# Kernel optimization log

Measured on AMD Instinct MI355X. Metric: run time of the kernel, lower is better.

Reference implementation:

```python
import jax, jax.numpy as jnp
import numpy as np


def _lambertw_real(z: float) -> float:
    # real branch W0 for z > e, Newton iteration (static, numpy)
    w = np.log(z) - np.log(np.log(z))
    for _ in range(30):
        ew = np.exp(w)
        w = w - (w * ew - z) / (ew * (w + 1.0))
    return float(w)


def setup_inputs() -> dict:
    key = jax.random.key(0)
    ks = jax.random.split(key, 8)
    B, D, Wd, Hd, heads = 4, 64, 48, 48, 4
    dh = D // heads
    return {
        "x": jax.random.normal(ks[0], (B, D, Wd, Hd), jnp.float32),
        "Wq": jax.random.normal(ks[1], (heads, dh, D), jnp.float32) * 0.05,
        "bq": jax.random.normal(ks[2], (heads, dh), jnp.float32) * 0.05,
        "Wv": jax.random.normal(ks[3], (heads, dh, D), jnp.float32) * 0.05,
        "bv": jax.random.normal(ks[4], (heads, dh), jnp.float32) * 0.05,
        "Wo": jax.random.normal(ks[5], (D, D), jnp.float32) * 0.05,
        "bo": jax.random.normal(ks[6], (D,), jnp.float32) * 0.05,
        "gamma": jax.random.normal(ks[7], (1,), jnp.float32),
    }


def reference(x, Wq, bq, Wv, bv, Wo, bo, gamma):
    B, D, Wd, Hd = x.shape
    heads, dh, _ = Wq.shape
    N = Wd * Hd
    scalar = jnp.sqrt(jnp.asarray(D / heads, jnp.float32))

    x_flat = x.reshape(B, D, N)          # true [B, D, N] layout (1x1 conv input)
    x_r = x.reshape(B, N, D)             # faithful to torch x.view(B, N, D)

    outs = []
    for h in range(heads):
        # q: [B, N, dh] (conv1x1 then permute)
        q = jnp.einsum('kd,bdn->bnk', Wq[h], x_flat) + bq[h][None, None, :]
        qn = jnp.sum(q * q, axis=2)      # squared row norms [B, N]
        # expanded squared L2 distance: ||qi||^2 - 2 qi.qj + ||qj||^2
        dist = qn[:, :, None] - 2.0 * jnp.einsum('bnk,bmk->bnm', q, q) + qn[:, None, :]
        P = jax.nn.softmax(dist / (-scalar), axis=-1)   # [B, N, N]
        # A_h from weight.view(1, D, dh): row-major reshape, NOT transpose
        WqR = Wq[h].reshape(D, dh)
        A = (WqR @ WqR.T) / scalar       # [D, D]
        f = jnp.einsum('bnm,bmd->bnd', P, x_r) @ A      # [B, N, D]
        f_img = f.reshape(B, D, N)       # faithful to .view(B, D, W, H)
        v = jnp.einsum('kd,bdn->bkn', Wv[h], f_img) + bv[h][None, :, None]
        outs.append(v.reshape(B, N, dh))  # faithful to .view(B, N, dh)

    cat = jnp.concatenate(outs, axis=2).reshape(B, D, N)  # .view(B, D, W, H)
    out = jnp.einsum('od,bdn->bon', Wo, cat) + bo[None, :, None]

    # Lipschitz-style bound
    phi = jnp.asarray(_lambertw_real(N / np.e), jnp.float32)
    term = jnp.sqrt(jnp.sum(jnp.sum(Wq * Wq, axis=(1, 2)) * jnp.sum(Wv * Wv, axis=(1, 2))))
    bound = jnp.sqrt(jnp.asarray(N / D, jnp.float32)) * (4.0 * phi + 1.0) * term * jnp.linalg.norm(Wo)

    out = out / bound
    return gamma * out.reshape(B, D, Wd, Hd) + x
```

## Files before the change

### kernel.cpp

```cpp
#include <hip/hip_runtime.h>
#include <math.h>


#define OFF_SC  0
#define OFF_AF  16
#define OFF_QFB 8208
#define OFF_QFA 303120
#define OFF_QN  598032
#define OFF_XF  634896
#define OFF_F2  929808

#define LOG2E 1.44269504f

typedef __attribute__((ext_vector_type(8))) short bf16x8;
typedef __attribute__((ext_vector_type(16))) float f32x16;
union U4 { uint4 u; bf16x8 b; };

__device__ __forceinline__ unsigned short f2bf(float x) {
    unsigned int u = __float_as_uint(x);
    unsigned int r = u + 0x7fffu + ((u >> 16) & 1u);
    return (unsigned short)(r >> 16);
}
__device__ __forceinline__ float bf2f(unsigned short v) {
    return __uint_as_float((unsigned int)v << 16);
}

__global__ __launch_bounds__(256) void k_prep(
    const float* __restrict__ x, const float* __restrict__ Wq,
    const float* __restrict__ bq, const float* __restrict__ Wv,
    const float* __restrict__ Wo, const float* __restrict__ gamma, float* ws)
{
    __shared__ __align__(16) char smem[8192];
    const int bid = blockIdx.x, t = threadIdx.x;

    if (bid == 0) {
        double* red  = (double*)smem;
        double* sums = (double*)(smem + 2048);
        for (int ph = 0; ph < 9; ++ph) {
            double s = 0.0;
            if (ph < 4) {
                const float* W = Wq + ph * 1024;
                for (int i = t; i < 1024; i += 256) { double v = W[i]; s += v * v; }
            } else if (ph < 8) {
                const float* W = Wv + (ph - 4) * 1024;
                for (int i = t; i < 1024; i += 256) { double v = W[i]; s += v * v; }
            } else {
                for (int i = t; i < 4096; i += 256) { double v = Wo[i]; s += v * v; }
            }
            red[t] = s; __syncthreads();
            for (int off = 128; off; off >>= 1) {
                if (t < off) red[t] += red[t + off];
                __syncthreads();
            }
            if (t == 0) sums[ph] = red[0];
            __syncthreads();
        }
        if (t == 0) {
            float z = 2304.0f / 2.7182818284590452f;
            float w = logf(z) - logf(logf(z));
            #pragma unroll 1
            for (int it = 0; it < 30; ++it) {
                float ew = __expf(w);
                w = w - (w * ew - z) / (ew * (w + 1.0f));
            }
            double phi = (double)w;
            double term = sqrt(sums[0]*sums[4] + sums[1]*sums[5] +
                               sums[2]*sums[6] + sums[3]*sums[7]);
            double bound = 6.0 * (4.0 * phi + 1.0) * term * sqrt(sums[8]);
            ws[OFF_SC] = (float)((double)gamma[0] / bound);
        }
    } else if (bid <= 64) {
        float* WlP = (float*)smem;
        int id = bid - 1, h = id >> 4, dq = id & 15;
        const float* W = Wq + h * 1024;
        for (int i = t; i < 1024; i += 256) WlP[(i >> 4) * 17 + (i & 15)] = W[i];
        __syncthreads();
        int dl = t >> 6, e = t & 63, d = dq * 4 + dl;
        float s = 0.f;
        #pragma unroll
        for (int k = 0; k < 16; ++k) s += WlP[d * 17 + k] * WlP[e * 17 + k];
        int tt = d >> 4, j = d & 7, l = ((d >> 3) & 1) * 32 + (e & 31), ec = e >> 5;
        unsigned short* af = (unsigned short*)(ws + OFF_AF);
        af[(((h * 4 + tt) * 2 + ec) * 64 + l) * 8 + j] = f2bf(0.25f * s);
    } else if (bid <= 640) {
        float* WlT = (float*)smem;
        float* bl  = (float*)(smem + 4096);
        float* qnp = (float*)(smem + 4160);
        int rb = bid - 65, bh = rb / 36, nb = rb % 36;
        int h = bh & 3, b = bh >> 2;
        const float* W = Wq + h * 1024;
        for (int i = t; i < 1024; i += 256) WlT[(i & 63) * 16 + (i >> 6)] = W[i];
        if (t < 16) bl[t] = bq[h * 16 + t];
        __syncthreads();
        int nl = t & 63, kg = t >> 6, n = nb * 64 + nl;
        const float* xb = x + (size_t)b * 147456;
        const float4* wrow = (const float4*)WlT;
        float q0 = bl[kg*4], q1 = bl[kg*4+1], q2 = bl[kg*4+2], q3 = bl[kg*4+3];
        for (int d = 0; d < 64; ++d) {
            float xv = xb[d * 2304 + n];
            float4 wv = wrow[d * 4 + kg];
            q0 = fmaf(wv.x, xv, q0); q1 = fmaf(wv.y, xv, q1);
            q2 = fmaf(wv.z, xv, q2); q3 = fmaf(wv.w, xv, q3);
        }
        qnp[kg * 64 + nl] = q0*q0 + q1*q1 + q2*q2 + q3*q3;
        unsigned pB0 = (unsigned)f2bf(q0) | ((unsigned)f2bf(q1) << 16);
        unsigned pB1 = (unsigned)f2bf(q2) | ((unsigned)f2bf(q3) << 16);
        const float sA = 0.5f * LOG2E;
        unsigned pA0 = (unsigned)f2bf(sA*q0) | ((unsigned)f2bf(sA*q1) << 16);
        unsigned pA1 = (unsigned)f2bf(sA*q2) | ((unsigned)f2bf(sA*q3) << 16);
        size_t base = (size_t)(bh * 72 + (n >> 5)) * 256
                    + (size_t)(((kg >> 1) * 32 + (n & 31)) * 4 + (kg & 1) * 2);
        *(uint2*)((unsigned*)((unsigned short*)(ws + OFF_QFB)) + base) = make_uint2(pB0, pB1);
        *(uint2*)((unsigned*)((unsigned short*)(ws + OFF_QFA)) + base) = make_uint2(pA0, pA1);
        __syncthreads();
        if (t < 64) {
            float qn = qnp[t] + qnp[64 + t] + qnp[128 + t] + qnp[192 + t];
            ws[OFF_QN + bh * 2304 + nb * 64 + t] = -0.25f * LOG2E * qn;
        }
    } else {
        int i = (bid - 641) * 256 + t;
        int l = i & 63, c1 = i >> 6;
        int dc = c1 & 1, c2 = c1 >> 1;
        int T = c2 % 144, b = c2 / 144;
        const float* xb = x + (size_t)b * 147456;
        int col = dc * 32 + (l & 31), mbase = 16 * T + (l >> 5) * 8;
        unsigned int pk[4];
        #pragma unroll
        for (int jj = 0; jj < 4; ++jj) {
            float f0 = xb[(mbase + 2*jj) * 64 + col];
            float f1 = xb[(mbase + 2*jj + 1) * 64 + col];
            pk[jj] = (unsigned int)f2bf(f0) | ((unsigned int)f2bf(f1) << 16);
        }
        ((uint4*)((unsigned short*)(ws + OFF_XF)))[i] = make_uint4(pk[0], pk[1], pk[2], pk[3]);
    }
}

__global__ __launch_bounds__(128, 3) void k_attn(float* __restrict__ ws)
{
    __shared__ __align__(16) float Ols[2][32][68];
    __shared__ float Lls[2][32];
    __shared__ __align__(16) unsigned short fls[32][80];

    const int t = threadIdx.x, w = t >> 6, lane = t & 63;
    const int bid = blockIdx.x, bh = bid / 72, rc = bid % 72;
    const int h = bh & 3;
    const int b = bh >> 2;
    const int hi = lane >> 5, nl = lane & 31, s4 = hi * 4;

    const uint4* QB = (const uint4*)((const unsigned short*)(ws + OFF_QFB)) + (size_t)bh * 4608;
    const uint4* QA = (const uint4*)((const unsigned short*)(ws + OFF_QFA)) + (size_t)bh * 4608;
    const uint4* XF = (const uint4*)((const unsigned short*)(ws + OFF_XF)) + (size_t)b * 18432;
    const float* qn = ws + OFF_QN + bh * 2304;

    U4 qb; qb.u = QB[rc * 64 + lane];
    const float qoffl = qn[rc * 32 + nl];

    f32x16 O0, O1;
    #pragma unroll
    for (int i = 0; i < 16; ++i) { O0[i] = 0.f; O1[i] = 0.f; }
    float lrun = 0.f;

    for (int mt = w; mt < 36; mt += 2) {
        const int m0 = mt * 64;
        U4 xv[8];
        #pragma unroll
        for (int q = 0; q < 8; ++q) xv[q].u = XF[(size_t)(mt * 8 + q) * 64 + lane];
        U4 a0, a1;
        a0.u = QA[(mt * 2) * 64 + lane];
        a1.u = QA[(mt * 2 + 1) * 64 + lane];
        f32x16 c0, c1;
        #pragma unroll
        for (int g = 0; g < 4; ++g) {
            float4 t4 = *(const float4*)(qn + m0 + 8 * g + s4);
            c0[4*g+0] = t4.x + qoffl; c0[4*g+1] = t4.y + qoffl;
            c0[4*g+2] = t4.z + qoffl; c0[4*g+3] = t4.w + qoffl;
            float4 u4 = *(const float4*)(qn + m0 + 32 + 8 * g + s4);
            c1[4*g+0] = u4.x + qoffl; c1[4*g+1] = u4.y + qoffl;
            c1[4*g+2] = u4.z + qoffl; c1[4*g+3] = u4.w + qoffl;
        }
        f32x16 s0 = __builtin_amdgcn_mfma_f32_32x32x16_bf16(a0.b, qb.b, c0, 0, 0, 0);
        f32x16 s1 = __builtin_amdgcn_mfma_f32_32x32x16_bf16(a1.b, qb.b, c1, 0, 0, 0);
        float p[32];
        #pragma unroll
        for (int r = 0; r < 16; ++r)
            asm("v_exp_f32 %0, %1" : "=v"(p[r]) : "v"(s0[r]));
        #pragma unroll
        for (int r = 0; r < 16; ++r)
            asm("v_exp_f32 %0, %1" : "=v"(p[16 + r]) : "v"(s1[r]));
        float la = 0.f, lb = 0.f, lc = 0.f, ld = 0.f;
        #pragma unroll
        for (int r = 0; r < 32; r += 4) {
            la += p[r]; lb += p[r+1]; lc += p[r+2]; ld += p[r+3];
        }
        lrun += (la + lb) + (lc + ld);
        #pragma unroll
        for (int c = 0; c < 2; ++c) {
            unsigned int wd[8], xd[8];
            #pragma unroll
            for (int i = 0; i < 8; ++i)
                asm("v_cvt_pk_bf16_f32 %0, %1, %2"
                    : "=v"(wd[i]) : "v"(p[c*16 + 2*i]), "v"(p[c*16 + 2*i + 1]));
            #pragma unroll
            for (int i = 0; i < 8; ++i) xd[i] = (unsigned int)__shfl_xor((int)wd[i], 32);
            U4 af0, af1;
            af0.u.x = hi ? xd[2] : wd[0];  af0.u.y = hi ? xd[3] : wd[1];
            af0.u.z = hi ? wd[2] : xd[0];  af0.u.w = hi ? wd[3] : xd[1];
            af1.u.x = hi ? xd[6] : wd[4];  af1.u.y = hi ? xd[7] : wd[5];
            af1.u.z = hi ? wd[6] : xd[4];  af1.u.w = hi ? wd[7] : xd[5];
            O0 = __builtin_amdgcn_mfma_f32_32x32x16_bf16(af0.b, xv[4*c+0].b, O0, 0, 0, 0);
            O1 = __builtin_amdgcn_mfma_f32_32x32x16_bf16(af0.b, xv[4*c+1].b, O1, 0, 0, 0);
            O0 = __builtin_amdgcn_mfma_f32_32x32x16_bf16(af1.b, xv[4*c+2].b, O0, 0, 0, 0);
            O1 = __builtin_amdgcn_mfma_f32_32x32x16_bf16(af1.b, xv[4*c+3].b, O1, 0, 0, 0);
        }
    }

    lrun += __shfl_xor(lrun, 32);
    #pragma unroll
    for (int r = 0; r < 16; ++r) {
        int n = (r & 3) + 8 * (r >> 2) + s4;
        Ols[w][n][nl]      = O0[r];
        Ols[w][n][nl + 32] = O1[r];
    }
    if (!hi) Lls[w][nl] = lrun;
    __syncthreads();

    {
        int n = t >> 2, ds = (t & 3) * 16;
        float invL = 1.f / (Lls[0][n] + Lls[1][n]);
        float f[16];
        #pragma unroll
        for (int j = 0; j < 16; ++j)
            f[j] = (Ols[0][n][ds + j] + Ols[1][n][ds + j]) * invL;
        unsigned int pk[8];
        #pragma unroll
        for (int i = 0; i < 8; ++i)
            asm("v_cvt_pk_bf16_f32 %0, %1, %2" : "=v"(pk[i]) : "v"(f[2*i]), "v"(f[2*i+1]));
        char* dst = (char*)&fls[0][0] + n * 160 + ds * 2;
        *(uint4*)(dst)      = make_uint4(pk[0], pk[1], pk[2], pk[3]);
        *(uint4*)(dst + 16) = make_uint4(pk[4], pk[5], pk[6], pk[7]);
    }
    __syncthreads();

    {
        const int ec = w;
        const uint4* AFp = (const uint4*)((const unsigned short*)(ws + OFF_AF)) + h * 512;
        f32x16 acc;
        #pragma unroll
        for (int i = 0; i < 16; ++i) acc[i] = 0.f;
        #pragma unroll
        for (int tt = 0; tt < 4; ++tt) {
            U4 a, bb;
            a.u  = *(const uint4*)((const char*)&fls[0][0] + nl * 160 + tt * 32 + hi * 16);
            bb.u = AFp[(tt * 2 + ec) * 64 + lane];
            acc = __builtin_amdgcn_mfma_f32_32x32x16_bf16(a.b, bb.b, acc, 0, 0, 0);
        }
        unsigned short* f2g = (unsigned short*)(ws + OFF_F2) +
                              (size_t)bh * 147456 + (size_t)rc * 32 * 64;
        #pragma unroll
        for (int r = 0; r < 16; ++r)
            f2g[((r & 3) + 8 * (r >> 2) + s4) * 64 + ec * 32 + nl] = f2bf(acc[r]);
    }
}

__global__ __launch_bounds__(256) void k_post(
    const float* __restrict__ x, const float* __restrict__ Wv,
    const float* __restrict__ bv, const float* __restrict__ Wo,
    const float* __restrict__ bo, const float* __restrict__ ws,
    float* __restrict__ out)
{
    __shared__ float WvL[4096];
    __shared__ float WoT[64 * 68];
    __shared__ float catL[16][68];
    __shared__ float bvL[64], boL[64];
    __shared__ float scs;
    const int bid = blockIdx.x, t = threadIdx.x;
    const int b = bid / 144, n0 = (bid % 144) * 16;
    for (int i = t; i < 4096; i += 256) WvL[i] = Wv[i];
    for (int i = t; i < 4096; i += 256) WoT[(i & 63) * 68 + (i >> 6)] = Wo[i];
    if (t < 64) { bvL[t] = bv[t]; boL[t] = bo[t]; }
    if (t == 0) scs = ws[OFF_SC];
    __syncthreads();

    const int nl = t & 15, q = t >> 4;
    const int n = n0 + nl;
    {
        const int h = q >> 2, cq = q & 3;
        const int k = n / 144;
        const int np = (n % 144) * 16 + cq * 4;
        const unsigned short* f2p = (const unsigned short*)(ws + OFF_F2)
                                  + (size_t)(b * 4 + h) * 147456;
        const float* wv = WvL + h * 1024 + k * 64;
        float bvv = bvL[h * 16 + k];
        float v0 = bvv, v1 = bvv, v2 = bvv, v3 = bvv;
        for (int d = 0; d < 64; ++d) {
            ushort4 f4 = *(const ushort4*)(f2p + d * 2304 + np);
            float wd = wv[d];
            v0 = fmaf(wd, bf2f(f4.x), v0);
            v1 = fmaf(wd, bf2f(f4.y), v1);
            v2 = fmaf(wd, bf2f(f4.z), v2);
            v3 = fmaf(wd, bf2f(f4.w), v3);
        }
        int col = h * 16 + cq * 4;
        catL[nl][col + 0] = v0; catL[nl][col + 1] = v1;
        catL[nl][col + 2] = v2; catL[nl][col + 3] = v3;
    }
    __syncthreads();
    {
        const int oq = q;
        const float4* wo4 = (const float4*)WoT;
        float a0 = boL[oq*4], a1 = boL[oq*4+1], a2 = boL[oq*4+2], a3 = boL[oq*4+3];
        for (int d = 0; d < 64; ++d) {
            float cv = catL[nl][d];
            float4 w4 = wo4[d * 17 + oq];
            a0 = fmaf(w4.x, cv, a0); a1 = fmaf(w4.y, cv, a1);
            a2 = fmaf(w4.z, cv, a2); a3 = fmaf(w4.w, cv, a3);
        }
        float sc = scs;
        const float* xb = x + (size_t)b * 147456;
        float* ob = out + (size_t)b * 147456;
        int o = oq * 4;
        ob[(o+0) * 2304 + n] = fmaf(sc, a0, xb[(o+0) * 2304 + n]);
        ob[(o+1) * 2304 + n] = fmaf(sc, a1, xb[(o+1) * 2304 + n]);
        ob[(o+2) * 2304 + n] = fmaf(sc, a2, xb[(o+2) * 2304 + n]);
        ob[(o+3) * 2304 + n] = fmaf(sc, a3, xb[(o+3) * 2304 + n]);
    }
}

extern "C" void kernel_launch(void* const* d_in, const int* in_sizes, int n_in,
                              void* d_out, int out_size, void* d_ws, size_t ws_size,
                              hipStream_t stream) {
    const float* x     = (const float*)d_in[0];
    const float* Wq    = (const float*)d_in[1];
    const float* bq    = (const float*)d_in[2];
    const float* Wv    = (const float*)d_in[3];
    const float* bv    = (const float*)d_in[4];
    const float* Wo    = (const float*)d_in[5];
    const float* bo    = (const float*)d_in[6];
    const float* gamma = (const float*)d_in[7];
    float* out = (float*)d_out;
    float* ws  = (float*)d_ws;
    k_prep<<<929,  256, 0, stream>>>(x, Wq, bq, Wv, Wo, gamma, ws);
    k_attn<<<1152, 128, 0, stream>>>(ws);
    k_post<<<576,  256, 0, stream>>>(x, Wv, bv, Wo, bo, ws, out);
}
```

Before: 133.4 us.

## Use four waves per attention block with double-buffered tile loads and LDS-staged norms

The attention kernel grows from two to four waves per block, each handling a quarter of the key tiles, and the four partial accumulators and row sums are reduced in shared memory. The main loop is fully unrolled and double-buffered, so each wave prefetches the next tile's X and Q fragments while computing the current tile. The squared norms are staged once into LDS instead of being read from global memory in every iteration. This aims to hide global load latency and add parallelism within each block, at the cost of higher register pressure from two fragment buffers, a larger shared-memory footprint and two waves idling during the final projection.

After: 129.7 us. 1.03x faster.

```diff
diff --git a/kernel.cpp b/kernel.cpp
--- a/kernel.cpp
+++ b/kernel.cpp
@@ -135,11 +135,70 @@
     }
 }
 
-__global__ __launch_bounds__(128, 3) void k_attn(float* __restrict__ ws)
+#define ATTN_TILE(XV, A0, A1, MT)                                               \
+    {                                                                           \
+        const int m0_ = (MT) * 64;                                              \
+        f32x16 c0_, c1_;                                                        \
+        _Pragma("unroll")                                                       \
+        for (int g = 0; g < 4; ++g) {                                           \
+            float4 t4_ = *(const float4*)(qn_s + m0_ + 8 * g + s4);             \
+            c0_[4*g+0] = t4_.x + qoffl; c0_[4*g+1] = t4_.y + qoffl;             \
+            c0_[4*g+2] = t4_.z + qoffl; c0_[4*g+3] = t4_.w + qoffl;             \
+            float4 u4_ = *(const float4*)(qn_s + m0_ + 32 + 8 * g + s4);        \
+            c1_[4*g+0] = u4_.x + qoffl; c1_[4*g+1] = u4_.y + qoffl;             \
+            c1_[4*g+2] = u4_.z + qoffl; c1_[4*g+3] = u4_.w + qoffl;             \
+        }                                                                       \
+        f32x16 s0_ = __builtin_amdgcn_mfma_f32_32x32x16_bf16((A0).b, qb.b, c0_, 0, 0, 0); \
+        f32x16 s1_ = __builtin_amdgcn_mfma_f32_32x32x16_bf16((A1).b, qb.b, c1_, 0, 0, 0); \
+        float p_[32];                                                           \
+        _Pragma("unroll")                                                       \
+        for (int r = 0; r < 16; ++r)                                            \
+            asm("v_exp_f32 %0, %1" : "=v"(p_[r]) : "v"(s0_[r]));                \
+        _Pragma("unroll")                                                       \
+        for (int r = 0; r < 16; ++r)                                            \
+            asm("v_exp_f32 %0, %1" : "=v"(p_[16 + r]) : "v"(s1_[r]));           \
+        float la_ = 0.f, lb_ = 0.f, lc_ = 0.f, ld_ = 0.f;                       \
+        _Pragma("unroll")                                                       \
+        for (int r = 0; r < 32; r += 4) {                                       \
+            la_ += p_[r]; lb_ += p_[r+1]; lc_ += p_[r+2]; ld_ += p_[r+3];       \
+        }                                                                       \
+        lrun += (la_ + lb_) + (lc_ + ld_);                                      \
+        _Pragma("unroll")                                                       \
+        for (int c = 0; c < 2; ++c) {                                           \
+            unsigned int wd_[8], xd_[8];                                        \
+            _Pragma("unroll")                                                   \
+            for (int i = 0; i < 8; ++i)                                         \
+                asm("v_cvt_pk_bf16_f32 %0, %1, %2"                              \
+                    : "=v"(wd_[i]) : "v"(p_[c*16 + 2*i]), "v"(p_[c*16 + 2*i + 1])); \
+            _Pragma("unroll")                                                   \
+            for (int i = 0; i < 8; ++i) xd_[i] = (unsigned int)__shfl_xor((int)wd_[i], 32); \
+            U4 af0_, af1_;                                                      \
+            af0_.u.x = hi ? xd_[2] : wd_[0];  af0_.u.y = hi ? xd_[3] : wd_[1];  \
+            af0_.u.z = hi ? wd_[2] : xd_[0];  af0_.u.w = hi ? wd_[3] : xd_[1];  \
+            af1_.u.x = hi ? xd_[6] : wd_[4];  af1_.u.y = hi ? xd_[7] : wd_[5];  \
+            af1_.u.z = hi ? wd_[6] : xd_[4];  af1_.u.w = hi ? wd_[7] : xd_[5];  \
+            O0 = __builtin_amdgcn_mfma_f32_32x32x16_bf16(af0_.b, (XV)[4*c+0].b, O0, 0, 0, 0); \
+            O1 = __builtin_amdgcn_mfma_f32_32x32x16_bf16(af0_.b, (XV)[4*c+1].b, O1, 0, 0, 0); \
+            O0 = __builtin_amdgcn_mfma_f32_32x32x16_bf16(af1_.b, (XV)[4*c+2].b, O0, 0, 0, 0); \
+            O1 = __builtin_amdgcn_mfma_f32_32x32x16_bf16(af1_.b, (XV)[4*c+3].b, O1, 0, 0, 0); \
+        }                                                                       \
+    }
+
+#define ATTN_LOAD(XV, A0, A1, MT)                                               \
+    {                                                                           \
+        _Pragma("unroll")                                                       \
+        for (int q = 0; q < 8; ++q) (XV)[q].u = XF[(size_t)((MT) * 8 + q) * 64 + lane]; \
+        (A0).u = QA[((MT) * 2) * 64 + lane];                                    \
+        (A1).u = QA[((MT) * 2 + 1) * 64 + lane];                                \
+    }
+
+__global__ __launch_bounds__(256, 2) void k_attn(float* __restrict__ ws)
 {
-    __shared__ __align__(16) float Ols[2][32][68];
-    __shared__ float Lls[2][32];
-    __shared__ __align__(16) unsigned short fls[32][80];
+    __shared__ __align__(16) char smem[40448];
+    float* qn_s = (float*)smem;
+    float (*Ols)[32][68] = (float (*)[32][68])smem;
+    unsigned short (*fls)[80] = (unsigned short (*)[80])(smem + 34816);
+    float* Lls = (float*)(smem + 34816 + 5120);
 
     const int t = threadIdx.x, w = t >> 6, lane = t & 63;
     const int bid = blockIdx.x, bh = bid / 72, rc = bid % 72;
@@ -152,6 +211,9 @@
     const uint4* XF = (const uint4*)((const unsigned short*)(ws + OFF_XF)) + (size_t)b * 18432;
     const float* qn = ws + OFF_QN + bh * 2304;
 
+    for (int i = t; i < 576; i += 256)
+        ((float4*)qn_s)[i] = ((const float4*)qn)[i];
+
     U4 qb; qb.u = QB[rc * 64 + lane];
     const float qoffl = qn[rc * 32 + nl];
 
@@ -160,59 +222,22 @@
     for (int i = 0; i < 16; ++i) { O0[i] = 0.f; O1[i] = 0.f; }
     float lrun = 0.f;
 
-    for (int mt = w; mt < 36; mt += 2) {
-        const int m0 = mt * 64;
-        U4 xv[8];
-        #pragma unroll
-        for (int q = 0; q < 8; ++q) xv[q].u = XF[(size_t)(mt * 8 + q) * 64 + lane];
-        U4 a0, a1;
-        a0.u = QA[(mt * 2) * 64 + lane];
-        a1.u = QA[(mt * 2 + 1) * 64 + lane];
-        f32x16 c0, c1;
-        #pragma unroll
-        for (int g = 0; g < 4; ++g) {
-            float4 t4 = *(const float4*)(qn + m0 + 8 * g + s4);
-            c0[4*g+0] = t4.x + qoffl; c0[4*g+1] = t4.y + qoffl;
-            c0[4*g+2] = t4.z + qoffl; c0[4*g+3] = t4.w + qoffl;
-            float4 u4 = *(const float4*)(qn + m0 + 32 + 8 * g + s4);
-            c1[4*g+0] = u4.x + qoffl; c1[4*g+1] = u4.y + qoffl;
-            c1[4*g+2] = u4.z + qoffl; c1[4*g+3] = u4.w + qoffl;
-        }
-        f32x16 s0 = __builtin_amdgcn_mfma_f32_32x32x16_bf16(a0.b, qb.b, c0, 0, 0, 0);
-        f32x16 s1 = __builtin_amdgcn_mfma_f32_32x32x16_bf16(a1.b, qb.b, c1, 0, 0, 0);
-        float p[32];
-        #pragma unroll
-        for (int r = 0; r < 16; ++r)
-            asm("v_exp_f32 %0, %1" : "=v"(p[r]) : "v"(s0[r]));
-        #pragma unroll
-        for (int r = 0; r < 16; ++r)
-            asm("v_exp_f32 %0, %1" : "=v"(p[16 + r]) : "v"(s1[r]));
-        float la = 0.f, lb = 0.f, lc = 0.f, ld = 0.f;
-        #pragma unroll
-        for (int r = 0; r < 32; r += 4) {
-            la += p[r]; lb += p[r+1]; lc += p[r+2]; ld += p[r+3];
-        }
-        lrun += (la + lb) + (lc + ld);
-        #pragma unroll
-        for (int c = 0; c < 2; ++c) {
-            unsigned int wd[8], xd[8];
-            #pragma unroll
-            for (int i = 0; i < 8; ++i)
-                asm("v_cvt_pk_bf16_f32 %0, %1, %2"
-                    : "=v"(wd[i]) : "v"(p[c*16 + 2*i]), "v"(p[c*16 + 2*i + 1]));
-            #pragma unroll
-            for (int i = 0; i < 8; ++i) xd[i] = (unsigned int)__shfl_xor((int)wd[i], 32);
-            U4 af0, af1;
-            af0.u.x = hi ? xd[2] : wd[0];  af0.u.y = hi ? xd[3] : wd[1];
-            af0.u.z = hi ? wd[2] : xd[0];  af0.u.w = hi ? wd[3] : xd[1];
-            af1.u.x = hi ? xd[6] : wd[4];  af1.u.y = hi ? xd[7] : wd[5];
-            af1.u.z = hi ? wd[6] : xd[4];  af1.u.w = hi ? wd[7] : xd[5];
-            O0 = __builtin_amdgcn_mfma_f32_32x32x16_bf16(af0.b, xv[4*c+0].b, O0, 0, 0, 0);
-            O1 = __builtin_amdgcn_mfma_f32_32x32x16_bf16(af0.b, xv[4*c+1].b, O1, 0, 0, 0);
-            O0 = __builtin_amdgcn_mfma_f32_32x32x16_bf16(af1.b, xv[4*c+2].b, O0, 0, 0, 0);
-            O1 = __builtin_amdgcn_mfma_f32_32x32x16_bf16(af1.b, xv[4*c+3].b, O1, 0, 0, 0);
-        }
-    }
+    U4 xvA[8], a0A, a1A, xvB[8], a0B, a1B;
+    ATTN_LOAD(xvA, a0A, a1A, w);
+    __syncthreads();
+
+    #pragma unroll
+    for (int it = 0; it < 9; ++it) {
+        const int mt = w + it * 4;
+        if (it & 1) {
+            if (it < 8) ATTN_LOAD(xvA, a0A, a1A, mt + 4);
+            ATTN_TILE(xvB, a0B, a1B, mt);
+        } else {
+            if (it < 8) ATTN_LOAD(xvB, a0B, a1B, mt + 4);
+            ATTN_TILE(xvA, a0A, a1A, mt);
+        }
+    }
+    __syncthreads();
 
     lrun += __shfl_xor(lrun, 32);
     #pragma unroll
@@ -221,27 +246,26 @@
         Ols[w][n][nl]      = O0[r];
         Ols[w][n][nl + 32] = O1[r];
     }
-    if (!hi) Lls[w][nl] = lrun;
+    if (!hi) Lls[w * 32 + nl] = lrun;
     __syncthreads();
 
     {
-        int n = t >> 2, ds = (t & 3) * 16;
-        float invL = 1.f / (Lls[0][n] + Lls[1][n]);
-        float f[16];
-        #pragma unroll
-        for (int j = 0; j < 16; ++j)
-            f[j] = (Ols[0][n][ds + j] + Ols[1][n][ds + j]) * invL;
-        unsigned int pk[8];
-        #pragma unroll
-        for (int i = 0; i < 8; ++i)
+        int n = t >> 3, d0 = (t & 7) * 8;
+        float invL = 1.f / (Lls[n] + Lls[32 + n] + Lls[64 + n] + Lls[96 + n]);
+        float f[8];
+        #pragma unroll
+        for (int j = 0; j < 8; ++j)
+            f[j] = (Ols[0][n][d0+j] + Ols[1][n][d0+j] +
+                    Ols[2][n][d0+j] + Ols[3][n][d0+j]) * invL;
+        unsigned int pk[4];
+        #pragma unroll
+        for (int i = 0; i < 4; ++i)
             asm("v_cvt_pk_bf16_f32 %0, %1, %2" : "=v"(pk[i]) : "v"(f[2*i]), "v"(f[2*i+1]));
-        char* dst = (char*)&fls[0][0] + n * 160 + ds * 2;
-        *(uint4*)(dst)      = make_uint4(pk[0], pk[1], pk[2], pk[3]);
-        *(uint4*)(dst + 16) = make_uint4(pk[4], pk[5], pk[6], pk[7]);
-    }
-    __syncthreads();
-
-    {
+        *(uint4*)((char*)&fls[0][0] + n * 160 + d0 * 2) = make_uint4(pk[0], pk[1], pk[2], pk[3]);
+    }
+    __syncthreads();
+
+    if (w < 2) {
         const int ec = w;
         const uint4* AFp = (const uint4*)((const unsigned short*)(ws + OFF_AF)) + h * 512;
         f32x16 acc;
@@ -340,6 +364,6 @@
     float* out = (float*)d_out;
     float* ws  = (float*)d_ws;
     k_prep<<<929,  256, 0, stream>>>(x, Wq, bq, Wv, Wo, gamma, ws);
-    k_attn<<<1152, 128, 0, stream>>>(ws);
+    k_attn<<<1152, 256, 0, stream>>>(ws);
     k_post<<<576,  256, 0, stream>>>(x, Wv, bv, Wo, bo, ws, out);
 }
```

## Split attention key loop across four waves with 32-row tiles and LDS qn

Applied to the files above, without the earlier changes.

The attention kernel now runs four waves per block instead of two. Each wave processes 32-key half tiles, so the per-wave loop keeps 18 iterations but does half the work per iteration. The squared norms qn are staged into shared memory, the block index is remapped to interleave groups of blocks, and the final reduction sums four partial accumulators. Shared memory is aliased between qn and the partial outputs. The change is meant to raise latency hiding and occupancy, at the cost of a larger LDS reduction, extra barriers, and idle waves in the projection epilogue.

Measured after the change: 131.9 us. No clear change (-1.1%).

```diff
diff --git a/kernel.cpp b/kernel.cpp
--- a/kernel.cpp
+++ b/kernel.cpp
@@ -135,14 +135,17 @@
     }
 }
 
-__global__ __launch_bounds__(128, 3) void k_attn(float* __restrict__ ws)
+__global__ __launch_bounds__(256, 4) void k_attn(float* __restrict__ ws)
 {
-    __shared__ __align__(16) float Ols[2][32][68];
-    __shared__ float Lls[2][32];
-    __shared__ __align__(16) unsigned short fls[32][80];
+    __shared__ __align__(16) char smem[40448];
+    float* qn_s = (float*)smem;
+    float (*Ols)[32][68] = (float (*)[32][68])smem;
+    unsigned short (*fls)[80] = (unsigned short (*)[80])(smem + 34816);
+    float* Lls = (float*)(smem + 34816 + 5120);
 
     const int t = threadIdx.x, w = t >> 6, lane = t & 63;
-    const int bid = blockIdx.x, bh = bid / 72, rc = bid % 72;
+    const int bid = (blockIdx.x & 7) * 144 + (blockIdx.x >> 3);
+    const int bh = bid / 72, rc = bid % 72;
     const int h = bh & 3;
     const int b = bh >> 2;
     const int hi = lane >> 5, nl = lane & 31, s4 = hi * 4;
@@ -152,6 +155,9 @@
     const uint4* XF = (const uint4*)((const unsigned short*)(ws + OFF_XF)) + (size_t)b * 18432;
     const float* qn = ws + OFF_QN + bh * 2304;
 
+    for (int i = t; i < 576; i += 256)
+        ((float4*)qn_s)[i] = ((const float4*)qn)[i];
+
     U4 qb; qb.u = QB[rc * 64 + lane];
     const float qoffl = qn[rc * 32 + nl];
 
@@ -160,59 +166,52 @@
     for (int i = 0; i < 16; ++i) { O0[i] = 0.f; O1[i] = 0.f; }
     float lrun = 0.f;
 
-    for (int mt = w; mt < 36; mt += 2) {
-        const int m0 = mt * 64;
-        U4 xv[8];
-        #pragma unroll
-        for (int q = 0; q < 8; ++q) xv[q].u = XF[(size_t)(mt * 8 + q) * 64 + lane];
-        U4 a0, a1;
-        a0.u = QA[(mt * 2) * 64 + lane];
-        a1.u = QA[(mt * 2 + 1) * 64 + lane];
-        f32x16 c0, c1;
+    __syncthreads();
+
+    #pragma unroll 2
+    for (int it = 0; it < 18; ++it) {
+        const int ht = w + it * 4;
+        const int m0 = ht * 32;
+        U4 xv[4];
+        #pragma unroll
+        for (int q = 0; q < 4; ++q) xv[q].u = XF[(size_t)(ht * 4 + q) * 64 + lane];
+        U4 a0; a0.u = QA[ht * 64 + lane];
+        f32x16 c0;
         #pragma unroll
         for (int g = 0; g < 4; ++g) {
-            float4 t4 = *(const float4*)(qn + m0 + 8 * g + s4);
+            float4 t4 = *(const float4*)(qn_s + m0 + 8 * g + s4);
             c0[4*g+0] = t4.x + qoffl; c0[4*g+1] = t4.y + qoffl;
             c0[4*g+2] = t4.z + qoffl; c0[4*g+3] = t4.w + qoffl;
-            float4 u4 = *(const float4*)(qn + m0 + 32 + 8 * g + s4);
-            c1[4*g+0] = u4.x + qoffl; c1[4*g+1] = u4.y + qoffl;
-            c1[4*g+2] = u4.z + qoffl; c1[4*g+3] = u4.w + qoffl;
         }
         f32x16 s0 = __builtin_amdgcn_mfma_f32_32x32x16_bf16(a0.b, qb.b, c0, 0, 0, 0);
-        f32x16 s1 = __builtin_amdgcn_mfma_f32_32x32x16_bf16(a1.b, qb.b, c1, 0, 0, 0);
-        float p[32];
+        float p[16];
         #pragma unroll
         for (int r = 0; r < 16; ++r)
             asm("v_exp_f32 %0, %1" : "=v"(p[r]) : "v"(s0[r]));
-        #pragma unroll
-        for (int r = 0; r < 16; ++r)
-            asm("v_exp_f32 %0, %1" : "=v"(p[16 + r]) : "v"(s1[r]));
         float la = 0.f, lb = 0.f, lc = 0.f, ld = 0.f;
         #pragma unroll
-        for (int r = 0; r < 32; r += 4) {
+        for (int r = 0; r < 16; r += 4) {
             la += p[r]; lb += p[r+1]; lc += p[r+2]; ld += p[r+3];
         }
         lrun += (la + lb) + (lc + ld);
-        #pragma unroll
-        for (int c = 0; c < 2; ++c) {
-            unsigned int wd[8], xd[8];
-            #pragma unroll
-            for (int i = 0; i < 8; ++i)
-                asm("v_cvt_pk_bf16_f32 %0, %1, %2"
-                    : "=v"(wd[i]) : "v"(p[c*16 + 2*i]), "v"(p[c*16 + 2*i + 1]));
-            #pragma unroll
-            for (int i = 0; i < 8; ++i) xd[i] = (unsigned int)__shfl_xor((int)wd[i], 32);
-            U4 af0, af1;
-            af0.u.x = hi ? xd[2] : wd[0];  af0.u.y = hi ? xd[3] : wd[1];
-            af0.u.z = hi ? wd[2] : xd[0];  af0.u.w = hi ? wd[3] : xd[1];
-            af1.u.x = hi ? xd[6] : wd[4];  af1.u.y = hi ? xd[7] : wd[5];
-            af1.u.z = hi ? wd[6] : xd[4];  af1.u.w = hi ? wd[7] : xd[5];
-            O0 = __builtin_amdgcn_mfma_f32_32x32x16_bf16(af0.b, xv[4*c+0].b, O0, 0, 0, 0);
-            O1 = __builtin_amdgcn_mfma_f32_32x32x16_bf16(af0.b, xv[4*c+1].b, O1, 0, 0, 0);
-            O0 = __builtin_amdgcn_mfma_f32_32x32x16_bf16(af1.b, xv[4*c+2].b, O0, 0, 0, 0);
-            O1 = __builtin_amdgcn_mfma_f32_32x32x16_bf16(af1.b, xv[4*c+3].b, O1, 0, 0, 0);
-        }
-    }
+        unsigned int wd[8], xd[8];
+        #pragma unroll
+        for (int i = 0; i < 8; ++i)
+            asm("v_cvt_pk_bf16_f32 %0, %1, %2"
+                : "=v"(wd[i]) : "v"(p[2*i]), "v"(p[2*i + 1]));
+        #pragma unroll
+        for (int i = 0; i < 8; ++i) xd[i] = (unsigned int)__shfl_xor((int)wd[i], 32);
+        U4 af0, af1;
+        af0.u.x = hi ? xd[2] : wd[0];  af0.u.y = hi ? xd[3] : wd[1];
+        af0.u.z = hi ? wd[2] : xd[0];  af0.u.w = hi ? wd[3] : xd[1];
+        af1.u.x = hi ? xd[6] : wd[4];  af1.u.y = hi ? xd[7] : wd[5];
+        af1.u.z = hi ? wd[6] : xd[4];  af1.u.w = hi ? wd[7] : xd[5];
+        O0 = __builtin_amdgcn_mfma_f32_32x32x16_bf16(af0.b, xv[0].b, O0, 0, 0, 0);
+        O1 = __builtin_amdgcn_mfma_f32_32x32x16_bf16(af0.b, xv[1].b, O1, 0, 0, 0);
+        O0 = __builtin_amdgcn_mfma_f32_32x32x16_bf16(af1.b, xv[2].b, O0, 0, 0, 0);
+        O1 = __builtin_amdgcn_mfma_f32_32x32x16_bf16(af1.b, xv[3].b, O1, 0, 0, 0);
+    }
+    __syncthreads();
 
     lrun += __shfl_xor(lrun, 32);
     #pragma unroll
@@ -221,27 +220,26 @@
         Ols[w][n][nl]      = O0[r];
         Ols[w][n][nl + 32] = O1[r];
     }
-    if (!hi) Lls[w][nl] = lrun;
+    if (!hi) Lls[w * 32 + nl] = lrun;
     __syncthreads();
 
     {
-        int n = t >> 2, ds = (t & 3) * 16;
-        float invL = 1.f / (Lls[0][n] + Lls[1][n]);
-        float f[16];
-        #pragma unroll
-        for (int j = 0; j < 16; ++j)
-            f[j] = (Ols[0][n][ds + j] + Ols[1][n][ds + j]) * invL;
-        unsigned int pk[8];
-        #pragma unroll
-        for (int i = 0; i < 8; ++i)
+        int n = t >> 3, d0 = (t & 7) * 8;
+        float invL = 1.f / (Lls[n] + Lls[32 + n] + Lls[64 + n] + Lls[96 + n]);
+        float f[8];
+        #pragma unroll
+        for (int j = 0; j < 8; ++j)
+            f[j] = (Ols[0][n][d0+j] + Ols[1][n][d0+j] +
+                    Ols[2][n][d0+j] + Ols[3][n][d0+j]) * invL;
+        unsigned int pk[4];
+        #pragma unroll
+        for (int i = 0; i < 4; ++i)
             asm("v_cvt_pk_bf16_f32 %0, %1, %2" : "=v"(pk[i]) : "v"(f[2*i]), "v"(f[2*i+1]));
-        char* dst = (char*)&fls[0][0] + n * 160 + ds * 2;
-        *(uint4*)(dst)      = make_uint4(pk[0], pk[1], pk[2], pk[3]);
-        *(uint4*)(dst + 16) = make_uint4(pk[4], pk[5], pk[6], pk[7]);
-    }
-    __syncthreads();
-
-    {
+        *(uint4*)((char*)&fls[0][0] + n * 160 + d0 * 2) = make_uint4(pk[0], pk[1], pk[2], pk[3]);
+    }
+    __syncthreads();
+
+    if (w < 2) {
         const int ec = w;
         const uint4* AFp = (const uint4*)((const unsigned short*)(ws + OFF_AF)) + h * 512;
         f32x16 acc;
@@ -340,6 +338,6 @@
     float* out = (float*)d_out;
     float* ws  = (float*)d_ws;
     k_prep<<<929,  256, 0, stream>>>(x, Wq, bq, Wv, Wo, gamma, ws);
-    k_attn<<<1152, 128, 0, stream>>>(ws);
+    k_attn<<<1152, 256, 0, stream>>>(ws);
     k_post<<<576,  256, 0, stream>>>(x, Wv, bv, Wo, bo, ws, out);
 }
```
